# Kernel tuning notes

Hardware: AMD Instinct MI355X
Metric: run time of the kernel (lower is better)

The kernel has to match this reference:

```python
import jax, jax.numpy as jnp
import numpy as np

N_NODES = 50000
N_EDGES = 600000
D = 128
EPS = 1e-12  # F.normalize eps


def setup_inputs() -> dict:
    key = jax.random.key(0)
    k1, k2, k3, k4, k5 = jax.random.split(key, 5)
    h = jax.random.normal(k1, (N_NODES, D), dtype=jnp.float32)
    snorm_n = jax.random.uniform(k2, (N_NODES, 1), dtype=jnp.float32)
    W = jax.random.normal(k3, (D, 2 * D), dtype=jnp.float32) * (1.0 / np.sqrt(2 * D))
    src = jax.random.randint(k4, (N_EDGES,), 0, N_NODES, dtype=jnp.int32)
    dst = jax.random.randint(k5, (N_EDGES,), 0, N_NODES, dtype=jnp.int32)
    return {"h": h, "snorm_n": snorm_n, "W": W, "src": src, "dst": dst}


def reference(h, snorm_n, W, src, dst):
    # message passing: gather src features, mean-reduce onto dst (DGL copy_src + mean)
    msg = h[src]                                               # [E, D]
    summed = jax.ops.segment_sum(msg, dst, num_segments=N_NODES)   # [N, D]
    deg = jax.ops.segment_sum(jnp.ones((N_EDGES,), h.dtype), dst, num_segments=N_NODES)
    c = summed / jnp.maximum(deg, 1.0)[:, None]                # zero for isolated nodes
    # NodeApply: concat(h, c) -> Linear(2D -> D, no bias) -> L2 normalize -> relu
    bundle = jnp.concatenate([h, c], axis=1) @ W.T             # [N, D]
    nrm = jnp.sqrt(jnp.sum(bundle * bundle, axis=1, keepdims=True))
    bundle = bundle / jnp.maximum(nrm, EPS)
    out = jax.nn.relu(bundle)
    # graph_norm
    return out * snorm_n
```

## Files before the change

kernel.cpp:

```cpp
#include <hip/hip_runtime.h>
#include <hip/hip_bf16.h>

#define N_NODES_C 50000
#define N_EDGES_C 600000
#define DIM 128
#define BCAP 64
#define BK2  48
#define NBINS 196
#define BINCAP 4096
#define EBLOCKS 2344
#define HCVT_BLOCKS 2048

#define P1_BLOCKS 256
#define P1_EPB 2344
#define M2CVT_BLOCKS 1024

typedef __attribute__((ext_vector_type(8))) short short8;
typedef __attribute__((ext_vector_type(4))) float f32x4;

__device__ inline unsigned short f2bf_u(float f) {
    union { __hip_bfloat16 b; unsigned short u; } cv;
    cv.b = __float2bfloat16(f);
    return cv.u;
}

__device__ inline short8 cvt8(const float* p) {
    const float4 lo = *reinterpret_cast<const float4*>(p);
    const float4 hi = *reinterpret_cast<const float4*>(p + 4);
    short8 r;
    r[0] = (short)f2bf_u(lo.x); r[1] = (short)f2bf_u(lo.y);
    r[2] = (short)f2bf_u(lo.z); r[3] = (short)f2bf_u(lo.w);
    r[4] = (short)f2bf_u(hi.x); r[5] = (short)f2bf_u(hi.y);
    r[6] = (short)f2bf_u(hi.z); r[7] = (short)f2bf_u(hi.w);
    return r;
}


__global__ void prepW_kernel(int* __restrict__ binCnt, const float4* __restrict__ W4,
                             ushort4* __restrict__ Wb4) {
    const int b = blockIdx.x;
    const int t = threadIdx.x;
    if (b == 0) {
        if (t < NBINS) binCnt[t] = 0;
    } else {
        const int i = (b - 1) * 256 + t;
        if (i < 8192) {
            const float4 v = W4[i];
            ushort4 o;
            o.x = f2bf_u(v.x); o.y = f2bf_u(v.y); o.z = f2bf_u(v.z); o.w = f2bf_u(v.w);
            Wb4[i] = o;
        }
    }
}


__global__ void mega2_kernel(const int* __restrict__ src, const int* __restrict__ dst,
                             int* __restrict__ binCnt, unsigned int* __restrict__ binned,
                             const float4* __restrict__ h4, ushort4* __restrict__ hb4) {
    __shared__ int hist[200];
    __shared__ int cursor[200];

    const int b = blockIdx.x;
    const int t = threadIdx.x;

    if (b < P1_BLOCKS) {
        const int start = b * P1_EPB;
        const int end   = min(start + P1_EPB, N_EDGES_C);
        if (t < 200) hist[t] = 0;
        __syncthreads();
        for (int e = start + t; e < end; e += 256)
            atomicAdd(&hist[dst[e] >> 8], 1);
        __syncthreads();
        if (t < NBINS) {
            const int c = hist[t];
            cursor[t] = (c > 0) ? atomicAdd(&binCnt[t], c) : 0;
        }
        __syncthreads();
        for (int e = start + t; e < end; e += 256) {
            const int d   = dst[e];
            const int bin = d >> 8;
            const int pos = atomicAdd(&cursor[bin], 1);
            if (pos < BINCAP)
                binned[bin * BINCAP + pos] =
                    (unsigned int)src[e] | ((unsigned int)(d & 255) << 16);
        }
    } else {
        const int n4 = N_NODES_C * DIM / 4;
        const int stride = M2CVT_BLOCKS * 256;
        for (int i = (b - P1_BLOCKS) * 256 + t; i < n4; i += stride) {
            const float4 v = h4[i];
            ushort4 o;
            o.x = f2bf_u(v.x); o.y = f2bf_u(v.y); o.z = f2bf_u(v.z); o.w = f2bf_u(v.w);
            hb4[i] = o;
        }
    }
}


__global__ void bucket_kernel(const int* __restrict__ binCnt,
                              const unsigned int* __restrict__ binned,
                              int* __restrict__ cnt, unsigned short* __restrict__ esrc2,
                              int nNodes) {
    __shared__ int cnt256[256];
    __shared__ unsigned short lb[256 * BK2];

    const int g = blockIdx.x;
    const int t = threadIdx.x;
    const int m = min(binCnt[g], BINCAP);

    cnt256[t] = 0;
    __syncthreads();

    for (int i = t; i < m; i += 256) {
        const unsigned int u = binned[g * BINCAP + i];
        const int n = (int)(u >> 16);
        const int p = atomicAdd(&cnt256[n], 1);
        if (p < BK2) lb[n * BK2 + p] = (unsigned short)(u & 0xFFFFu);
    }
    __syncthreads();

    const int node = g * 256 + t;
    if (node < nNodes) {
        const int dg  = cnt256[t];
        cnt[node] = dg;
        const int dgs = (dg < BK2) ? dg : BK2;
        for (int i = 0; i < dgs; ++i)
            esrc2[node * BCAP + i] = lb[t * BK2 + i];
    }
}


__global__ void agg4_bf_kernel(const unsigned short* __restrict__ hb,
                               const int* __restrict__ cnt,
                               const unsigned short* __restrict__ esrc2,
                               unsigned short* __restrict__ cb, int nNodes) {
    const int tid  = threadIdx.x;
    const int lane = tid & 63;
    const int wid  = tid >> 6;
    const int node = blockIdx.x * 4 + wid;
    if (node >= nNodes) return;

    const int dg  = cnt[node];
    const int dgs = (dg < BK2) ? dg : BK2;
    const int c8  = lane & 15;
    const int eq  = lane >> 4;

    const int ev  = (lane < dgs) ? (int)esrc2[node * BCAP + lane] : 0;
    const int nit = (dgs + 3) >> 2;

    float a0 = 0.f, a1 = 0.f, a2 = 0.f, a3 = 0.f;
    float a4 = 0.f, a5 = 0.f, a6 = 0.f, a7 = 0.f;
    for (int it = 0; it < nit; ++it) {
        const int e = 4 * it + eq;
        const int s = __shfl(ev, e);
        if (e < dgs) {
            const uint4 u = *reinterpret_cast<const uint4*>(hb + s * DIM + c8 * 8);
            a0 += __uint_as_float(u.x << 16);
            a1 += __uint_as_float(u.x & 0xffff0000u);
            a2 += __uint_as_float(u.y << 16);
            a3 += __uint_as_float(u.y & 0xffff0000u);
            a4 += __uint_as_float(u.z << 16);
            a5 += __uint_as_float(u.z & 0xffff0000u);
            a6 += __uint_as_float(u.w << 16);
            a7 += __uint_as_float(u.w & 0xffff0000u);
        }
    }
    a0 += __shfl_xor(a0, 16); a1 += __shfl_xor(a1, 16);
    a2 += __shfl_xor(a2, 16); a3 += __shfl_xor(a3, 16);
    a4 += __shfl_xor(a4, 16); a5 += __shfl_xor(a5, 16);
    a6 += __shfl_xor(a6, 16); a7 += __shfl_xor(a7, 16);
    a0 += __shfl_xor(a0, 32); a1 += __shfl_xor(a1, 32);
    a2 += __shfl_xor(a2, 32); a3 += __shfl_xor(a3, 32);
    a4 += __shfl_xor(a4, 32); a5 += __shfl_xor(a5, 32);
    a6 += __shfl_xor(a6, 32); a7 += __shfl_xor(a7, 32);

    if (lane < 16) {
        const float inv = 1.0f / (float)(dg > 1 ? dg : 1);
        uint4 o;
        o.x = (unsigned)f2bf_u(a0 * inv) | ((unsigned)f2bf_u(a1 * inv) << 16);
        o.y = (unsigned)f2bf_u(a2 * inv) | ((unsigned)f2bf_u(a3 * inv) << 16);
        o.z = (unsigned)f2bf_u(a4 * inv) | ((unsigned)f2bf_u(a5 * inv) << 16);
        o.w = (unsigned)f2bf_u(a6 * inv) | ((unsigned)f2bf_u(a7 * inv) << 16);
        *reinterpret_cast<uint4*>(cb + node * DIM + c8 * 8) = o;
    }
}


__launch_bounds__(256, 3)
__global__ void final4_kernel(const unsigned short* __restrict__ hb,
                              const unsigned short* __restrict__ cb,
                              const float* __restrict__ snorm,
                              const unsigned short* __restrict__ Wb,
                              float* __restrict__ out, int nNodes) {
    __shared__ float rowsq[2][16][4];

    const int tid  = threadIdx.x;
    const int wid  = tid >> 6;
    const int lane = tid & 63;
    const int lr   = lane & 15;
    const int lk   = lane >> 4;
    const int base = blockIdx.x * 32;

    short8 b[2][8];
#pragma unroll
    for (int t = 0; t < 2; ++t) {
        const int wrow = (wid * 2 + t) * 16 + lr;
#pragma unroll
        for (int ks = 0; ks < 8; ++ks)
            b[t][ks] = *reinterpret_cast<const short8*>(Wb + wrow * 256 + ks * 32 + lk * 8);
    }
#pragma unroll
    for (int t = 0; t < 2; ++t)
#pragma unroll
        for (int ks = 0; ks < 8; ++ks)
            asm volatile("" : "+v"(b[t][ks]));

    f32x4 acc[2][2];
#pragma unroll
    for (int rt = 0; rt < 2; ++rt) {
        acc[rt][0] = (f32x4)(0.f);
        acc[rt][1] = (f32x4)(0.f);
        int arow = base + rt * 16 + lr;
        arow = (arow < nNodes) ? arow : (nNodes - 1);
        const unsigned short* hp = hb + arow * DIM + lk * 8;
        const unsigned short* cp = cb + arow * DIM + lk * 8;

        short8 a[8];
#pragma unroll
        for (int ks = 0; ks < 4; ++ks) {
            a[ks]     = *reinterpret_cast<const short8*>(hp + ks * 32);
            a[ks + 4] = *reinterpret_cast<const short8*>(cp + ks * 32);
        }
#pragma unroll
        for (int ks = 0; ks < 8; ++ks) {
            acc[rt][0] = __builtin_amdgcn_mfma_f32_16x16x32_bf16(a[ks], b[0][ks], acc[rt][0], 0, 0, 0);
            acc[rt][1] = __builtin_amdgcn_mfma_f32_16x16x32_bf16(a[ks], b[1][ks], acc[rt][1], 0, 0, 0);
        }
#pragma unroll
        for (int r = 0; r < 4; ++r) {
            float sq = acc[rt][0][r] * acc[rt][0][r] + acc[rt][1][r] * acc[rt][1][r];
            sq += __shfl_xor(sq, 1);
            sq += __shfl_xor(sq, 2);
            sq += __shfl_xor(sq, 4);
            sq += __shfl_xor(sq, 8);
            if (lr == 0) rowsq[rt][lk * 4 + r][wid] = sq;
        }
    }
    __syncthreads();

#pragma unroll
    for (int rt = 0; rt < 2; ++rt) {
#pragma unroll
        for (int r = 0; r < 4; ++r) {
            const int row16 = lk * 4 + r;
            const int node  = base + rt * 16 + row16;
            if (node < nNodes) {
                const float nsq = rowsq[rt][row16][0] + rowsq[rt][row16][1]
                                + rowsq[rt][row16][2] + rowsq[rt][row16][3];
                const float scale = 1.0f / fmaxf(sqrtf(nsq), 1e-12f);
                const float sn    = snorm[node];
#pragma unroll
                for (int t = 0; t < 2; ++t) {
                    const int col = (wid * 2 + t) * 16 + lr;
                    out[node * DIM + col] = fmaxf(acc[rt][t][r] * scale, 0.f) * sn;
                }
            }
        }
    }
}


__global__ void prep_kernel(int4* __restrict__ cnt4, const float4* __restrict__ W4,
                            ushort4* __restrict__ Wb4, int doCvt) {
    const int b = blockIdx.x;
    const int t = threadIdx.x;
    if (b < 49) {
        const int i = b * 256 + t;
        if (i < 12500) cnt4[i] = make_int4(0, 0, 0, 0);
    } else if (doCvt) {
        const int i = (b - 49) * 256 + t;
        if (i < 8192) {
            const float4 v = W4[i];
            ushort4 o;
            o.x = f2bf_u(v.x); o.y = f2bf_u(v.y); o.z = f2bf_u(v.z); o.w = f2bf_u(v.w);
            Wb4[i] = o;
        }
    }
}

__global__ void fill2_kernel(const int* __restrict__ src, const int* __restrict__ dst,
                             int* __restrict__ cnt, unsigned short* __restrict__ esrc2,
                             const float4* __restrict__ h4, ushort4* __restrict__ hb4,
                             int doCvt) {
    const int b = blockIdx.x;
    const int t = threadIdx.x;
    if (b < EBLOCKS) {
        const int e = b * 256 + t;
        if (e < N_EDGES_C) {
            const int d   = dst[e];
            const int pos = atomicAdd(&cnt[d], 1);
            if (pos < BCAP) esrc2[d * BCAP + pos] = (unsigned short)src[e];
        }
    } else if (doCvt) {
        const int n4 = N_NODES_C * DIM / 4;
        int i = (b - EBLOCKS) * 256 + t;
        const int stride = HCVT_BLOCKS * 256;
        for (; i < n4; i += stride) {
            const float4 v = h4[i];
            ushort4 o;
            o.x = f2bf_u(v.x); o.y = f2bf_u(v.y); o.z = f2bf_u(v.z); o.w = f2bf_u(v.w);
            hb4[i] = o;
        }
    }
}

__global__ void agg2_bf_kernel(const unsigned short* __restrict__ hb,
                               const int* __restrict__ cnt,
                               const unsigned short* __restrict__ esrc2,
                               float* __restrict__ cout, int nNodes) {
    const int tid  = threadIdx.x;
    const int lane = tid & 63;
    const int wid  = tid >> 6;
    const int node = blockIdx.x * 4 + wid;
    if (node >= nNodes) return;

    const int dg  = cnt[node];
    const int dgs = (dg < BCAP) ? dg : BCAP;
    const int col4 = lane & 31;
    const int eh   = lane >> 5;

    const int ev = (lane < dgs) ? (int)esrc2[node * BCAP + lane] : 0;

    float4 acc = {0.f, 0.f, 0.f, 0.f};
    for (int it = 0; 2 * it + eh < dgs; ++it) {
        const int s = __shfl(ev, 2 * it + eh);
        const uint2 u = *reinterpret_cast<const uint2*>(hb + s * DIM + col4 * 4);
        acc.x += __uint_as_float(u.x << 16);
        acc.y += __uint_as_float(u.x & 0xffff0000u);
        acc.z += __uint_as_float(u.y << 16);
        acc.w += __uint_as_float(u.y & 0xffff0000u);
    }
    acc.x += __shfl_xor(acc.x, 32);
    acc.y += __shfl_xor(acc.y, 32);
    acc.z += __shfl_xor(acc.z, 32);
    acc.w += __shfl_xor(acc.w, 32);

    if (lane < 32) {
        const float inv = 1.0f / (float)(dg > 1 ? dg : 1);
        float4 o = {acc.x * inv, acc.y * inv, acc.z * inv, acc.w * inv};
        *reinterpret_cast<float4*>(cout + node * DIM + col4 * 4) = o;
    }
}

__launch_bounds__(256, 3)
__global__ void gemm2_bf_kernel(const unsigned short* __restrict__ hb,
                                const float* cfp,
                                const float* __restrict__ snorm,
                                const unsigned short* __restrict__ Wb,
                                float* out, int nNodes) {
    __shared__ float rowsq[2][16][4];

    const int tid  = threadIdx.x;
    const int wid  = tid >> 6;
    const int lane = tid & 63;
    const int lr   = lane & 15;
    const int lk   = lane >> 4;
    const int base = blockIdx.x * 32;

    short8 b[2][8];
#pragma unroll
    for (int t = 0; t < 2; ++t) {
        const int wrow = (wid * 2 + t) * 16 + lr;
#pragma unroll
        for (int ks = 0; ks < 8; ++ks)
            b[t][ks] = *reinterpret_cast<const short8*>(Wb + wrow * 256 + ks * 32 + lk * 8);
    }
#pragma unroll
    for (int t = 0; t < 2; ++t)
#pragma unroll
        for (int ks = 0; ks < 8; ++ks)
            asm volatile("" : "+v"(b[t][ks]));

    f32x4 acc[2][2];
#pragma unroll
    for (int rt = 0; rt < 2; ++rt) {
        acc[rt][0] = (f32x4)(0.f);
        acc[rt][1] = (f32x4)(0.f);
        int arow = base + rt * 16 + lr;
        arow = (arow < nNodes) ? arow : (nNodes - 1);
        const unsigned short* hp = hb + arow * DIM + lk * 8;
        const float*          cp = cfp + arow * DIM + lk * 8;

        short8 a[8];
#pragma unroll
        for (int ks = 0; ks < 4; ++ks)
            a[ks] = *reinterpret_cast<const short8*>(hp + ks * 32);
#pragma unroll
        for (int ks = 0; ks < 4; ++ks)
            a[ks + 4] = cvt8(cp + ks * 32);
#pragma unroll
        for (int ks = 0; ks < 8; ++ks) {
            acc[rt][0] = __builtin_amdgcn_mfma_f32_16x16x32_bf16(a[ks], b[0][ks], acc[rt][0], 0, 0, 0);
            acc[rt][1] = __builtin_amdgcn_mfma_f32_16x16x32_bf16(a[ks], b[1][ks], acc[rt][1], 0, 0, 0);
        }
#pragma unroll
        for (int r = 0; r < 4; ++r) {
            float sq = acc[rt][0][r] * acc[rt][0][r] + acc[rt][1][r] * acc[rt][1][r];
            sq += __shfl_xor(sq, 1);
            sq += __shfl_xor(sq, 2);
            sq += __shfl_xor(sq, 4);
            sq += __shfl_xor(sq, 8);
            if (lr == 0) rowsq[rt][lk * 4 + r][wid] = sq;
        }
    }
    __syncthreads();

#pragma unroll
    for (int rt = 0; rt < 2; ++rt) {
#pragma unroll
        for (int r = 0; r < 4; ++r) {
            const int row16 = lk * 4 + r;
            const int node  = base + rt * 16 + row16;
            if (node < nNodes) {
                const float nsq = rowsq[rt][row16][0] + rowsq[rt][row16][1]
                                + rowsq[rt][row16][2] + rowsq[rt][row16][3];
                const float scale = 1.0f / fmaxf(sqrtf(nsq), 1e-12f);
                const float sn    = snorm[node];
#pragma unroll
                for (int t = 0; t < 2; ++t) {
                    const int col = (wid * 2 + t) * 16 + lr;
                    out[node * DIM + col] = fmaxf(acc[rt][t][r] * scale, 0.f) * sn;
                }
            }
        }
    }
}


extern "C" void kernel_launch(void* const* d_in, const int* in_sizes, int n_in,
                              void* d_out, int out_size, void* d_ws, size_t ws_size,
                              hipStream_t stream) {
    const float* h     = (const float*)d_in[0];
    const float* snorm = (const float*)d_in[1];
    const float* W     = (const float*)d_in[2];
    const int*   src   = (const int*)d_in[3];
    const int*   dst   = (const int*)d_in[4];
    float*       out   = (float*)d_out;

    char* ws = (char*)d_ws;
    int*            cnt   = (int*)(ws + 0);
    unsigned short* esrc2 = (unsigned short*)(ws + 200064);
    unsigned short* hb    = (unsigned short*)(ws + 6600064);
    unsigned short* Wb    = (unsigned short*)(ws + 19400064);
    unsigned short* cb    = (unsigned short*)(ws + 19465600);
    int*            binCnt = (int*)(ws + 19465600);
    unsigned int*   binned = (unsigned int*)(ws + 19466624);
    const size_t NEED_A = 32265600;
    const size_t NEED_9 = 19465600;
    const int doCvt = (ws_size >= NEED_9) ? 1 : 0;

    if (ws_size >= NEED_A) {
        prepW_kernel<<<33, 256, 0, stream>>>(binCnt, (const float4*)W, (ushort4*)Wb);
        mega2_kernel<<<P1_BLOCKS + M2CVT_BLOCKS, 256, 0, stream>>>(
            src, dst, binCnt, binned, (const float4*)h, (ushort4*)hb);
        bucket_kernel<<<NBINS, 256, 0, stream>>>(binCnt, binned, cnt, esrc2, N_NODES_C);
        agg4_bf_kernel<<<(N_NODES_C + 3) / 4, 256, 0, stream>>>(hb, cnt, esrc2, cb, N_NODES_C);
        final4_kernel<<<(N_NODES_C + 31) / 32, 256, 0, stream>>>(hb, cb, snorm, Wb, out, N_NODES_C);
    } else {
        prep_kernel<<<81, 256, 0, stream>>>((int4*)cnt, (const float4*)W, (ushort4*)Wb, doCvt);
        fill2_kernel<<<EBLOCKS + (doCvt ? HCVT_BLOCKS : 0), 256, 0, stream>>>(
            src, dst, cnt, esrc2, (const float4*)h, (ushort4*)hb, doCvt);
        agg2_bf_kernel<<<(N_NODES_C + 3) / 4, 256, 0, stream>>>(hb, cnt, esrc2, out, N_NODES_C);
        gemm2_bf_kernel<<<(N_NODES_C + 31) / 32, 256, 0, stream>>>(hb, out, snorm, Wb, out, N_NODES_C);
    }
}
```

Baseline: 92.88 us.

## Replace global-atomic binning with per-block segment buckets and drop prep kernel

Edge binning now writes each block's edges into a private fixed-capacity segment per (bin, block) and records per-segment counts. This removes the separate histogram pass, the global atomics on bin counters and the zeroing kernel, and the W conversion is folded into the same launch. The bucket kernel has each thread walk one segment serially and writes esrc2 rows with 16-byte vector stores. The risks are silent edge loss if any block-bin segment exceeds 48 entries, and serial per-thread loads with poor coalescing in the bucket pass.

```diff
diff --git a/kernel.cpp b/kernel.cpp
--- a/kernel.cpp
+++ b/kernel.cpp
@@ -7,13 +7,14 @@
 #define BCAP 64
 #define BK2  48
 #define NBINS 196
-#define BINCAP 4096
+#define SEGCAP 48
 #define EBLOCKS 2344
 #define HCVT_BLOCKS 2048
 
 #define P1_BLOCKS 256
 #define P1_EPB 2344
-#define M2CVT_BLOCKS 1024
+#define WCVT_BLOCKS 32
+#define M3CVT_BLOCKS 1024
 
 typedef __attribute__((ext_vector_type(8))) short short8;
 typedef __attribute__((ext_vector_type(4))) float f32x4;
@@ -36,58 +37,42 @@
 }
 
 
-__global__ void prepW_kernel(int* __restrict__ binCnt, const float4* __restrict__ W4,
-                             ushort4* __restrict__ Wb4) {
+__global__ void mega3_kernel(const int* __restrict__ src, const int* __restrict__ dst,
+                             int* __restrict__ segCnt, unsigned int* __restrict__ binned,
+                             const float4* __restrict__ h4, ushort4* __restrict__ hb4,
+                             const float4* __restrict__ W4, ushort4* __restrict__ Wb4) {
+    __shared__ int cur[200];
+
     const int b = blockIdx.x;
     const int t = threadIdx.x;
-    if (b == 0) {
-        if (t < NBINS) binCnt[t] = 0;
-    } else {
-        const int i = (b - 1) * 256 + t;
+
+    if (b < P1_BLOCKS) {
+        const int start = b * P1_EPB;
+        const int end   = min(start + P1_EPB, N_EDGES_C);
+        if (t < 200) cur[t] = 0;
+        __syncthreads();
+        for (int e = start + t; e < end; e += 256) {
+            const int d   = dst[e];
+            const int bin = d >> 8;
+            const int pos = atomicAdd(&cur[bin], 1);
+            if (pos < SEGCAP)
+                binned[(bin * P1_BLOCKS + b) * SEGCAP + pos] =
+                    (unsigned int)src[e] | ((unsigned int)(d & 255) << 16);
+        }
+        __syncthreads();
+        if (t < NBINS) segCnt[b * NBINS + t] = cur[t];
+    } else if (b < P1_BLOCKS + WCVT_BLOCKS) {
+        const int i = (b - P1_BLOCKS) * 256 + t;
         if (i < 8192) {
             const float4 v = W4[i];
             ushort4 o;
             o.x = f2bf_u(v.x); o.y = f2bf_u(v.y); o.z = f2bf_u(v.z); o.w = f2bf_u(v.w);
             Wb4[i] = o;
         }
-    }
-}
-
-
-__global__ void mega2_kernel(const int* __restrict__ src, const int* __restrict__ dst,
-                             int* __restrict__ binCnt, unsigned int* __restrict__ binned,
-                             const float4* __restrict__ h4, ushort4* __restrict__ hb4) {
-    __shared__ int hist[200];
-    __shared__ int cursor[200];
-
-    const int b = blockIdx.x;
-    const int t = threadIdx.x;
-
-    if (b < P1_BLOCKS) {
-        const int start = b * P1_EPB;
-        const int end   = min(start + P1_EPB, N_EDGES_C);
-        if (t < 200) hist[t] = 0;
-        __syncthreads();
-        for (int e = start + t; e < end; e += 256)
-            atomicAdd(&hist[dst[e] >> 8], 1);
-        __syncthreads();
-        if (t < NBINS) {
-            const int c = hist[t];
-            cursor[t] = (c > 0) ? atomicAdd(&binCnt[t], c) : 0;
-        }
-        __syncthreads();
-        for (int e = start + t; e < end; e += 256) {
-            const int d   = dst[e];
-            const int bin = d >> 8;
-            const int pos = atomicAdd(&cursor[bin], 1);
-            if (pos < BINCAP)
-                binned[bin * BINCAP + pos] =
-                    (unsigned int)src[e] | ((unsigned int)(d & 255) << 16);
-        }
     } else {
         const int n4 = N_NODES_C * DIM / 4;
-        const int stride = M2CVT_BLOCKS * 256;
-        for (int i = (b - P1_BLOCKS) * 256 + t; i < n4; i += stride) {
+        const int stride = M3CVT_BLOCKS * 256;
+        for (int i = (b - P1_BLOCKS - WCVT_BLOCKS) * 256 + t; i < n4; i += stride) {
             const float4 v = h4[i];
             ushort4 o;
             o.x = f2bf_u(v.x); o.y = f2bf_u(v.y); o.z = f2bf_u(v.z); o.w = f2bf_u(v.w);
@@ -97,35 +82,39 @@
 }
 
 
-__global__ void bucket_kernel(const int* __restrict__ binCnt,
-                              const unsigned int* __restrict__ binned,
-                              int* __restrict__ cnt, unsigned short* __restrict__ esrc2,
-                              int nNodes) {
+__global__ void bucket2_kernel(const int* __restrict__ segCnt,
+                               const unsigned int* __restrict__ binned,
+                               int* __restrict__ cnt, unsigned short* __restrict__ esrc2,
+                               int nNodes) {
     __shared__ int cnt256[256];
     __shared__ unsigned short lb[256 * BK2];
 
     const int g = blockIdx.x;
     const int t = threadIdx.x;
-    const int m = min(binCnt[g], BINCAP);
 
     cnt256[t] = 0;
     __syncthreads();
 
-    for (int i = t; i < m; i += 256) {
-        const unsigned int u = binned[g * BINCAP + i];
+    const int c = min(segCnt[t * NBINS + g], SEGCAP);
+    const unsigned int* seg = binned + (g * P1_BLOCKS + t) * SEGCAP;
+    for (int i = 0; i < c; ++i) {
+        const unsigned int u = seg[i];
         const int n = (int)(u >> 16);
         const int p = atomicAdd(&cnt256[n], 1);
         if (p < BK2) lb[n * BK2 + p] = (unsigned short)(u & 0xFFFFu);
     }
     __syncthreads();
 
-    const int node = g * 256 + t;
-    if (node < nNodes) {
-        const int dg  = cnt256[t];
-        cnt[node] = dg;
-        const int dgs = (dg < BK2) ? dg : BK2;
-        for (int i = 0; i < dgs; ++i)
-            esrc2[node * BCAP + i] = lb[t * BK2 + i];
+    const int node0 = g * 256;
+    if (node0 + t < nNodes) cnt[node0 + t] = cnt256[t];
+
+    const uint4* lb4 = reinterpret_cast<const uint4*>(lb);
+    for (int f = t; f < 256 * 6; f += 256) {
+        const int n  = f / 6;
+        const int ch = f - n * 6;
+        if (node0 + n < nNodes)
+            *reinterpret_cast<uint4*>(esrc2 + (size_t)(node0 + n) * BCAP + ch * 8) =
+                lb4[n * 6 + ch];
     }
 }
 
@@ -453,17 +442,17 @@
     unsigned short* hb    = (unsigned short*)(ws + 6600064);
     unsigned short* Wb    = (unsigned short*)(ws + 19400064);
     unsigned short* cb    = (unsigned short*)(ws + 19465600);
-    int*            binCnt = (int*)(ws + 19465600);
-    unsigned int*   binned = (unsigned int*)(ws + 19466624);
+    unsigned int*   binned = (unsigned int*)(ws + 19465600);
+    int*            segCnt = (int*)(ws + 29099392);
     const size_t NEED_A = 32265600;
     const size_t NEED_9 = 19465600;
     const int doCvt = (ws_size >= NEED_9) ? 1 : 0;
 
     if (ws_size >= NEED_A) {
-        prepW_kernel<<<33, 256, 0, stream>>>(binCnt, (const float4*)W, (ushort4*)Wb);
-        mega2_kernel<<<P1_BLOCKS + M2CVT_BLOCKS, 256, 0, stream>>>(
-            src, dst, binCnt, binned, (const float4*)h, (ushort4*)hb);
-        bucket_kernel<<<NBINS, 256, 0, stream>>>(binCnt, binned, cnt, esrc2, N_NODES_C);
+        mega3_kernel<<<P1_BLOCKS + WCVT_BLOCKS + M3CVT_BLOCKS, 256, 0, stream>>>(
+            src, dst, segCnt, binned, (const float4*)h, (ushort4*)hb,
+            (const float4*)W, (ushort4*)Wb);
+        bucket2_kernel<<<NBINS, 256, 0, stream>>>(segCnt, binned, cnt, esrc2, N_NODES_C);
         agg4_bf_kernel<<<(N_NODES_C + 3) / 4, 256, 0, stream>>>(hb, cnt, esrc2, cb, N_NODES_C);
         final4_kernel<<<(N_NODES_C + 31) / 32, 256, 0, stream>>>(hb, cb, snorm, Wb, out, N_NODES_C);
     } else {
```

Result: faster. 83.95 us (-9.6%).
